# Kernel tuning notes

Measured on AMD Instinct MI355X. Metric: run time of the kernel, lower is better.

## Reference

```python
import jax, jax.numpy as jnp
import numpy as np

B, S, D, H, HID = 4, 1024, 1024, 16, 4096
DK = D // H
EPS = 1e-6


def _ln(x):
    # LayerNorm without affine, eps=1e-6
    mu = jnp.mean(x, axis=-1, keepdims=True)
    var = jnp.var(x, axis=-1, keepdims=True)
    return (x - mu) / jnp.sqrt(var + EPS)


def _lin(x, W, b):
    # torch Linear convention: W is [out, in]
    y = jnp.einsum('...i,oi->...o', x, W)
    return y + b if b is not None else y


def setup_inputs() -> dict:
    key = jax.random.key(0)
    ks = jax.random.split(key, 16)
    sc = lambda fan_in: 1.0 / np.sqrt(fan_in)
    inp = {
        'x': jax.random.normal(ks[0], (B, S, D), jnp.float32),
        'cond': jax.random.normal(ks[1], (B, 1, D), jnp.float32),
        'Wq': jax.random.normal(ks[2], (D, D), jnp.float32) * sc(D),
        'bq': jnp.zeros((D,), jnp.float32),
        'Wk': jax.random.normal(ks[3], (D, D), jnp.float32) * sc(D),
        'bk': jnp.zeros((D,), jnp.float32),
        'Wv': jax.random.normal(ks[4], (D, D), jnp.float32) * sc(D),
        'bv': jnp.zeros((D,), jnp.float32),
        'Wo': jax.random.normal(ks[5], (D, D), jnp.float32) * sc(D),
        'bo': jnp.zeros((D,), jnp.float32),
        'W1': jax.random.normal(ks[6], (HID, D), jnp.float32) * sc(D),
        'b1': jnp.zeros((HID,), jnp.float32),
        'W2': jax.random.normal(ks[7], (D, HID), jnp.float32) * sc(HID),
        'b2': jnp.zeros((D,), jnp.float32),
        'Wada': jax.random.normal(ks[8], (6 * D, D), jnp.float32) * sc(D),
        'bada': jnp.zeros((6 * D,), jnp.float32),
    }
    return inp


def reference(x, cond, Wq, bq, Wk, bk, Wv, bv, Wo, bo, W1, b1, W2, b2, Wada, bada):
    # adaLN modulation: SiLU -> Linear -> chunk 6 along last dim
    mod = _lin(jax.nn.silu(cond), Wada, bada)  # [B,1,6D]
    gama1, beta1, alpha1, gama2, beta2, alpha2 = jnp.split(mod, 6, axis=-1)

    # attention branch
    residual = x
    h = _ln(x) * (1.0 + beta1) + gama1  # modulate(shift=gama1, scale=beta1)
    q = _lin(h, Wq, bq).reshape(B, S, H, DK)
    k = _lin(h, Wk, bk).reshape(B, S, H, DK)
    v = _lin(h, Wv, bv).reshape(B, S, H, DK)
    scores = jnp.einsum('bqhd,bkhd->bhqk', q, k) / jnp.sqrt(jnp.float32(DK))
    probs = jax.nn.softmax(scores, axis=-1)
    attn = jnp.einsum('bhqk,bkhd->bqhd', probs, v).reshape(B, S, D)
    attn = _lin(attn, Wo, bo)
    x = residual + alpha1 * attn

    # MLP branch
    residual = x
    h = _ln(x) * (1.0 + beta2) + gama2
    h = _lin(h, W1, b1)
    h = jax.nn.gelu(h, approximate=False)  # torch nn.GELU default (erf)
    h = _lin(h, W2, b2)
    return residual + alpha2 * h
```

## Files before the change

### kernel.cpp

```cpp
#include <hip/hip_runtime.h>
#include <cstdint>

typedef __bf16 bf16_t;
typedef __bf16 bf16x4 __attribute__((ext_vector_type(4)));
typedef __bf16 bf16x8 __attribute__((ext_vector_type(8)));
typedef float f32x4 __attribute__((ext_vector_type(4)));

#define B_ 4
#define S_ 1024
#define D_ 1024
#define HID_ 4096
#define MEG (1u << 20)

static const size_t OFF_WBF  = 0;
static const size_t OFF_BQKV = 25165824;
static const size_t OFF_MOD  = 25178112;
static const size_t OFF_H    = 25276416;
static const size_t OFF_QKV  = 33665024;
static const size_t OFF_VT   = 58830848;
static const size_t OFF_ATTN = 67219456;
static const size_t OFF_X1   = 75608064;
static const size_t OFF_PART = 92385280;
static const size_t OFF_MLPH = 159494144;

__device__ __forceinline__ void async_copy16(const bf16_t* g, bf16_t* l) {
  __builtin_amdgcn_global_load_lds(
      (__attribute__((address_space(1))) void*)(g),
      (__attribute__((address_space(3))) void*)(l), 16, 0, 0);
}

__global__ __launch_bounds__(256) void convert_pack(
    const float* __restrict__ Wq, const float* __restrict__ Wk,
    const float* __restrict__ Wv, const float* __restrict__ Wo,
    const float* __restrict__ W1, const float* __restrict__ W2,
    const float* __restrict__ bq, const float* __restrict__ bk,
    const float* __restrict__ bv, bf16_t* __restrict__ wbf,
    float* __restrict__ bqkv) {
  const int y = blockIdx.y;
  if (y == 6) {
    int i = blockIdx.x * 256 + threadIdx.x;
    if (i < 3072)
      bqkv[i] = i < 1024 ? bq[i] : (i < 2048 ? bk[i - 1024] : bv[i - 2048]);
    return;
  }
  const float* src; bf16_t* dst; int n;
  switch (y) {
    case 0: src = Wq; dst = wbf;           n = MEG;     break;
    case 1: src = Wk; dst = wbf + MEG;     n = MEG;     break;
    case 2: src = Wv; dst = wbf + 2*MEG;   n = MEG;     break;
    case 3: src = Wo; dst = wbf + 3*MEG;   n = MEG;     break;
    case 4: src = W1; dst = wbf + 4*MEG;   n = 4*MEG;   break;
    default: src = W2; dst = wbf + 8*MEG;  n = 4*MEG;   break;
  }
  int idx = (blockIdx.x * 256 + threadIdx.x) * 4;
  if (idx < n) {
    float4 v = *(const float4*)(src + idx);
    bf16x4 pk;
    pk.x = (__bf16)v.x; pk.y = (__bf16)v.y; pk.z = (__bf16)v.z; pk.w = (__bf16)v.w;
    *(bf16x4*)(dst + idx) = pk;
  }
}

__global__ __launch_bounds__(256) void ada_mod(
    const float* __restrict__ cond, const float* __restrict__ Wada,
    const float* __restrict__ bada, float* __restrict__ mod) {
  const int wave = threadIdx.x >> 6, lane = threadIdx.x & 63;
  const int o = blockIdx.x * 4 + wave;
  const float* wr = Wada + (size_t)o * D_;
  float a0 = 0.f, a1 = 0.f, a2 = 0.f, a3 = 0.f;
#pragma unroll
  for (int l = 0; l < 16; l++) {
    int i = l * 64 + lane;
    float w = wr[i];
    float c0 = cond[i], c1 = cond[1024 + i], c2 = cond[2048 + i], c3 = cond[3072 + i];
    a0 += w * (c0 / (1.0f + __expf(-c0)));
    a1 += w * (c1 / (1.0f + __expf(-c1)));
    a2 += w * (c2 / (1.0f + __expf(-c2)));
    a3 += w * (c3 / (1.0f + __expf(-c3)));
  }
#pragma unroll
  for (int offs = 32; offs; offs >>= 1) {
    a0 += __shfl_xor(a0, offs);
    a1 += __shfl_xor(a1, offs);
    a2 += __shfl_xor(a2, offs);
    a3 += __shfl_xor(a3, offs);
  }
  if (lane == 0) {
    float bb = bada[o];
    mod[o]          = a0 + bb;
    mod[6144 + o]   = a1 + bb;
    mod[12288 + o]  = a2 + bb;
    mod[18432 + o]  = a3 + bb;
  }
}

__global__ __launch_bounds__(256) void ln_modulate(
    const float* __restrict__ X, const float* __restrict__ mod,
    bf16_t* __restrict__ H, int goff) {
  const int row = blockIdx.x;
  const int b = row >> 10;
  const int t = threadIdx.x;
  const float* xr = X + (size_t)row * D_;
  float4 xv = *(const float4*)(xr + t * 4);
  float s = xv.x + xv.y + xv.z + xv.w;
  float q = xv.x*xv.x + xv.y*xv.y + xv.z*xv.z + xv.w*xv.w;
  const int wave = t >> 6, lane = t & 63;
#pragma unroll
  for (int offs = 32; offs; offs >>= 1) {
    s += __shfl_down(s, offs);
    q += __shfl_down(q, offs);
  }
  __shared__ float sb[4][2];
  if (lane == 0) { sb[wave][0] = s; sb[wave][1] = q; }
  __syncthreads();
  float st = sb[0][0] + sb[1][0] + sb[2][0] + sb[3][0];
  float qt = sb[0][1] + sb[1][1] + sb[2][1] + sb[3][1];
  float mu = st * (1.0f / D_);
  float var = qt * (1.0f / D_) - mu * mu;
  float rstd = rsqrtf(var + 1e-6f);
  const float* mb = mod + (size_t)b * 6144 + goff;
  const int c = t * 4;
  float4 gm = *(const float4*)(mb + c);
  float4 bt = *(const float4*)(mb + 1024 + c);
  bf16x4 pk;
  pk.x = (__bf16)((xv.x - mu) * rstd * (1.0f + bt.x) + gm.x);
  pk.y = (__bf16)((xv.y - mu) * rstd * (1.0f + bt.y) + gm.y);
  pk.z = (__bf16)((xv.z - mu) * rstd * (1.0f + bt.z) + gm.z);
  pk.w = (__bf16)((xv.w - mu) * rstd * (1.0f + bt.w) + gm.w);
  *(bf16x4*)(H + (size_t)row * D_ + c) = pk;
}

__global__ __launch_bounds__(256) void transpose_v(
    const bf16_t* __restrict__ qkv, bf16_t* __restrict__ vT) {
  __shared__ bf16_t tile[64][65];
  const int bh = blockIdx.y;
  const int b = bh >> 4, hh = bh & 15;
  const int s0 = blockIdx.x * 64;
  const int t = threadIdx.x;
  const int tx = t & 63, ty = t >> 6;
  const bf16_t* src = qkv + (size_t)b * S_ * 3072 + 2048 + hh * 64;
  for (int r = ty; r < 64; r += 4)
    tile[r][tx] = src[(size_t)(s0 + r) * 3072 + tx];
  __syncthreads();
  bf16_t* dst = vT + (size_t)bh * 64 * 1024;
  for (int r = ty; r < 64; r += 4)
    dst[(size_t)r * 1024 + s0 + tx] = tile[tx][r];
}

__global__ __launch_bounds__(256) void flash_attn(
    const bf16_t* __restrict__ qkv, const bf16_t* __restrict__ vT,
    bf16_t* __restrict__ attn) {
  __shared__ __align__(16) bf16_t Qs[64 * 64];
  __shared__ __align__(16) bf16_t Ks[128 * 64];
  __shared__ __align__(16) bf16_t Vs[64 * 128];
  __shared__ __align__(16) bf16_t Ps[4 * 16 * 136];

  const int t = threadIdx.x;
  const int wave = t >> 6, lane = t & 63;
  const int lm = lane & 15, quad = lane >> 4;
  const int bh = blockIdx.y;
  const int b = bh >> 4, hh = bh & 15;
  const int s0 = blockIdx.x * 64;

  const bf16_t* qbase = qkv + (size_t)b * S_ * 3072 + hh * 64;
  const bf16_t* kbase = qbase + 1024;
  const bf16_t* vbase = vT + (size_t)bh * (64 * 1024);

#pragma unroll
  for (int j = 0; j < 2; j++) {
    int slot = j * 256 + t;
    int row = slot >> 3;
    int cg = (slot & 7) ^ (row & 7);
    async_copy16(qbase + (size_t)(s0 + row) * 3072 + cg * 8, &Qs[slot * 8]);
  }

  f32x4 accO[4] = {};
  float mrow[4], lrow[4];
#pragma unroll
  for (int r = 0; r < 4; r++) { mrow[r] = -1e30f; lrow[r] = 0.f; }

  bf16_t* Pw = &Ps[wave * 16 * 136];

  for (int k0 = 0; k0 < S_; k0 += 128) {
    __syncthreads();
#pragma unroll
    for (int j = 0; j < 4; j++) {
      int slot = j * 256 + t;
      int row = slot >> 3;
      int cg = (slot & 7) ^ (row & 7);
      async_copy16(kbase + (size_t)(k0 + row) * 3072 + cg * 8, &Ks[slot * 8]);
    }
#pragma unroll
    for (int j = 0; j < 4; j++) {
      int slot = j * 256 + t;
      int row = slot >> 4;
      int cp = slot & 15;
      int cg = (cp & 8) | ((cp & 7) ^ (row & 7));
      async_copy16(vbase + (size_t)row * 1024 + k0 + cg * 8, &Vs[slot * 8]);
    }
    __syncthreads();

    f32x4 accS[8] = {};
#pragma unroll
    for (int ks = 0; ks < 2; ks++) {
      int rq = wave * 16 + lm;
      int cq = (ks * 4 + quad) ^ (rq & 7);
      bf16x8 aq = *(const bf16x8*)&Qs[rq * 64 + cq * 8];
#pragma unroll
      for (int ni = 0; ni < 8; ni++) {
        int rk = ni * 16 + lm;
        int ck = (ks * 4 + quad) ^ (rk & 7);
        bf16x8 bk8 = *(const bf16x8*)&Ks[rk * 64 + ck * 8];
        accS[ni] = __builtin_amdgcn_mfma_f32_16x16x32_bf16(aq, bk8, accS[ni], 0, 0, 0);
      }
    }

    float alpha[4];
#pragma unroll
    for (int r = 0; r < 4; r++) {
      float mx = accS[0][r];
#pragma unroll
      for (int ni = 1; ni < 8; ni++) mx = fmaxf(mx, accS[ni][r]);
      mx = fmaxf(mx, __shfl_xor(mx, 1));
      mx = fmaxf(mx, __shfl_xor(mx, 2));
      mx = fmaxf(mx, __shfl_xor(mx, 4));
      mx = fmaxf(mx, __shfl_xor(mx, 8));
      mx *= 0.125f;
      float mnew = fmaxf(mrow[r], mx);
      alpha[r] = __expf(mrow[r] - mnew);
      mrow[r] = mnew;
      float sum = 0.f;
#pragma unroll
      for (int ni = 0; ni < 8; ni++) {
        float p = __expf(accS[ni][r] * 0.125f - mnew);
        accS[ni][r] = p;
        sum += p;
      }
      sum += __shfl_xor(sum, 1);
      sum += __shfl_xor(sum, 2);
      sum += __shfl_xor(sum, 4);
      sum += __shfl_xor(sum, 8);
      lrow[r] = lrow[r] * alpha[r] + sum;
    }
#pragma unroll
    for (int di = 0; di < 4; di++)
#pragma unroll
      for (int r = 0; r < 4; r++) accO[di][r] *= alpha[r];

#pragma unroll
    for (int ni = 0; ni < 8; ni++)
#pragma unroll
      for (int r = 0; r < 4; r++)
        Pw[(quad * 4 + r) * 136 + ni * 16 + lm] = (__bf16)accS[ni][r];

#pragma unroll
    for (int ks2 = 0; ks2 < 4; ks2++) {
      bf16x8 ap = *(const bf16x8*)&Pw[lm * 136 + ks2 * 32 + quad * 8];
#pragma unroll
      for (int di = 0; di < 4; di++) {
        int rv = di * 16 + lm;
        int g = ks2 * 4 + quad;
        int cp = (g & 8) | ((g & 7) ^ (rv & 7));
        bf16x8 bv = *(const bf16x8*)&Vs[rv * 128 + cp * 8];
        accO[di] = __builtin_amdgcn_mfma_f32_16x16x32_bf16(ap, bv, accO[di], 0, 0, 0);
      }
    }
  }

#pragma unroll
  for (int r = 0; r < 4; r++) {
    float inv = 1.0f / lrow[r];
    int row = quad * 4 + r;
#pragma unroll
    for (int di = 0; di < 4; di++) {
      int col = di * 16 + lm;
      int cph = (col >> 3) ^ (row & 7);
      Pw[row * 64 + cph * 8 + (col & 7)] = (__bf16)(accO[di][r] * inv);
    }
  }
  bf16_t* abase = attn + (size_t)b * S_ * 1024 +
                  (size_t)(s0 + wave * 16) * 1024 + hh * 64;
#pragma unroll
  for (int it = 0; it < 2; it++) {
    int slot = it * 64 + lane;
    int row = slot >> 3;
    int cg = slot & 7;
    int cph = cg ^ (row & 7);
    bf16x8 val = *(const bf16x8*)&Pw[row * 64 + cph * 8];
    *(bf16x8*)(abase + (size_t)row * 1024 + cg * 8) = val;
  }
}

template <int EPI>
__global__ __launch_bounds__(256) void gemm_bt(
    const bf16_t* __restrict__ A, int lda, long long sAz,
    const bf16_t* __restrict__ B, int ldb, long long sBz,
    void* __restrict__ Cv, int ldc, long long sCz,
    int M, int N, int K,
    const float* __restrict__ bias,
    float scale) {
  __shared__ __align__(16) bf16_t As[2][128 * 32];
  __shared__ __align__(16) bf16_t Bs[2][128 * 32];

  const int z = blockIdx.z;
  A += (size_t)z * sAz;
  B += (size_t)z * sBz;

  {
    int d = blockIdx.x + gridDim.x * blockIdx.y;
    int xcd = d & 7, sId = d >> 3;
    int qq = sId & 31, panel = sId >> 5;
    const int bx = panel * 8 + (qq >> 2);
    const int by = xcd * 4 + (qq & 3);
    const int t = threadIdx.x;
    const int wave = t >> 6;
    const int lane = t & 63;
    const int lm = lane & 15;
    const int quad = lane >> 4;
    const int wr = wave >> 1;
    const int wc = wave & 1;

    const int m0 = by * 128;
    const int n0 = bx * 128;

    f32x4 acc[4][4] = {};

    const int srow = t >> 2;
    const int gch = (t & 3) ^ ((srow >> 1) & 3);
    const int lds_off = t * 8;
    const bf16_t* Ap0 = A + (size_t)(m0 + srow) * lda + gch * 8;
    const bf16_t* Ap1 = A + (size_t)(m0 + 64 + srow) * lda + gch * 8;
    const bf16_t* Bp0 = B + (size_t)(n0 + srow) * ldb + gch * 8;
    const bf16_t* Bp1 = B + (size_t)(n0 + 64 + srow) * ldb + gch * 8;

    const int sOff = (quad ^ ((lm >> 1) & 3)) * 8;

    const int niter = K >> 5;
    async_copy16(Ap0, &As[0][lds_off]);
    async_copy16(Ap1, &As[0][2048 + lds_off]);
    async_copy16(Bp0, &Bs[0][lds_off]);
    async_copy16(Bp1, &Bs[0][2048 + lds_off]);

    for (int it = 0; it < niter; ++it) {
      asm volatile("s_waitcnt vmcnt(0)\n\ts_barrier" ::: "memory");
      if (it + 1 < niter) {
        const int ko = (it + 1) << 5;
        const int nb = (it + 1) & 1;
        async_copy16(Ap0 + ko, &As[nb][lds_off]);
        async_copy16(Ap1 + ko, &As[nb][2048 + lds_off]);
        async_copy16(Bp0 + ko, &Bs[nb][lds_off]);
        async_copy16(Bp1 + ko, &Bs[nb][2048 + lds_off]);
      }
      const int cb = it & 1;
      bf16x8 af[4], bfr[4];
#pragma unroll
      for (int i = 0; i < 4; i++) {
        af[i] = *(const bf16x8*)&As[cb][(wr * 64 + i * 16 + lm) * 32 + sOff];
        bfr[i] = *(const bf16x8*)&Bs[cb][(wc * 64 + i * 16 + lm) * 32 + sOff];
      }
#pragma unroll
      for (int mi = 0; mi < 4; mi++)
#pragma unroll
        for (int ni = 0; ni < 4; ni++)
          acc[mi][ni] = __builtin_amdgcn_mfma_f32_16x16x32_bf16(
              af[mi], bfr[ni], acc[mi][ni], 0, 0, 0);
    }

    const size_t cz = (size_t)z * sCz;
#pragma unroll
    for (int mi = 0; mi < 4; mi++) {
#pragma unroll
      for (int ni = 0; ni < 4; ni++) {
#pragma unroll
        for (int r = 0; r < 4; r++) {
          int row = m0 + wr * 64 + mi * 16 + quad * 4 + r;
          int col = n0 + wc * 64 + ni * 16 + lm;
          float v = acc[mi][ni][r];
          size_t idx = cz + (size_t)row * ldc + col;
          if (EPI == 1) {
            ((float*)Cv)[idx] = v * scale;
          } else if (EPI == 0) {
            if (bias) v += bias[col];
            ((bf16_t*)Cv)[idx] = (__bf16)v;
          } else if (EPI == 3) {
            v += bias[col];
            float u = 1.5957691216f * (v + 0.044715f * v * v * v);
            float g = v / (1.0f + __expf(-u));
            ((bf16_t*)Cv)[idx] = (__bf16)g;
          }
        }
      }
    }
  }
}

__global__ __launch_bounds__(256) void reduce_ln(
    const float* __restrict__ part, const float* __restrict__ x,
    const float* __restrict__ bo, const float* __restrict__ mod,
    float* __restrict__ x1, bf16_t* __restrict__ h) {
  const int row = blockIdx.x;
  const int b = row >> 10;
  const int t = threadIdx.x;
  const int c = t * 4;
  const size_t idx = (size_t)row * 1024 + c;
  float4 p0 = *(const float4*)(part + idx);
  float4 p1 = *(const float4*)(part + 4194304 + idx);
  float4 bb = *(const float4*)(bo + c);
  float4 al = *(const float4*)(mod + (size_t)b * 6144 + 2048 + c);
  float4 xs = *(const float4*)(x + idx);
  float4 xv;
  xv.x = xs.x + al.x * (p0.x + p1.x + bb.x);
  xv.y = xs.y + al.y * (p0.y + p1.y + bb.y);
  xv.z = xs.z + al.z * (p0.z + p1.z + bb.z);
  xv.w = xs.w + al.w * (p0.w + p1.w + bb.w);
  *(float4*)(x1 + idx) = xv;

  float s = xv.x + xv.y + xv.z + xv.w;
  float q = xv.x*xv.x + xv.y*xv.y + xv.z*xv.z + xv.w*xv.w;
  const int wave = t >> 6, lane = t & 63;
#pragma unroll
  for (int offs = 32; offs; offs >>= 1) {
    s += __shfl_down(s, offs);
    q += __shfl_down(q, offs);
  }
  __shared__ float sb[4][2];
  if (lane == 0) { sb[wave][0] = s; sb[wave][1] = q; }
  __syncthreads();
  float st = sb[0][0] + sb[1][0] + sb[2][0] + sb[3][0];
  float qt = sb[0][1] + sb[1][1] + sb[2][1] + sb[3][1];
  float mu = st * (1.0f / D_);
  float var = qt * (1.0f / D_) - mu * mu;
  float rstd = rsqrtf(var + 1e-6f);
  const float* mb = mod + (size_t)b * 6144 + 3072;
  float4 gm = *(const float4*)(mb + c);
  float4 bt = *(const float4*)(mb + 1024 + c);
  bf16x4 pk;
  pk.x = (__bf16)((xv.x - mu) * rstd * (1.0f + bt.x) + gm.x);
  pk.y = (__bf16)((xv.y - mu) * rstd * (1.0f + bt.y) + gm.y);
  pk.z = (__bf16)((xv.z - mu) * rstd * (1.0f + bt.z) + gm.z);
  pk.w = (__bf16)((xv.w - mu) * rstd * (1.0f + bt.w) + gm.w);
  *(bf16x4*)(h + idx) = pk;
}

__global__ __launch_bounds__(256) void reduce_w2(
    const float* __restrict__ part, const float* __restrict__ x1,
    const float* __restrict__ b2, const float* __restrict__ mod,
    float* __restrict__ out) {
  const int idx = (blockIdx.x * 256 + threadIdx.x) * 4;
  const int col = idx & 1023;
  const int row = idx >> 10;
  const int b = row >> 10;
  float4 s0 = *(const float4*)(part + idx);
  float4 s1 = *(const float4*)(part + 4194304 + idx);
  float4 bb = *(const float4*)(b2 + col);
  float4 al = *(const float4*)(mod + (size_t)b * 6144 + 5120 + col);
  float4 rs = *(const float4*)(x1 + idx);
  float4 o;
  o.x = rs.x + al.x * (s0.x + s1.x + bb.x);
  o.y = rs.y + al.y * (s0.y + s1.y + bb.y);
  o.z = rs.z + al.z * (s0.z + s1.z + bb.z);
  o.w = rs.w + al.w * (s0.w + s1.w + bb.w);
  *(float4*)(out + idx) = o;
}

extern "C" void kernel_launch(void* const* d_in, const int* in_sizes, int n_in,
                              void* d_out, int out_size, void* d_ws, size_t ws_size,
                              hipStream_t stream) {
  (void)in_sizes; (void)n_in; (void)out_size; (void)ws_size;
  const float* x    = (const float*)d_in[0];
  const float* cond = (const float*)d_in[1];
  const float* Wq   = (const float*)d_in[2];
  const float* bq   = (const float*)d_in[3];
  const float* Wk   = (const float*)d_in[4];
  const float* bk   = (const float*)d_in[5];
  const float* Wv   = (const float*)d_in[6];
  const float* bv   = (const float*)d_in[7];
  const float* Wo   = (const float*)d_in[8];
  const float* bo   = (const float*)d_in[9];
  const float* W1   = (const float*)d_in[10];
  const float* b1   = (const float*)d_in[11];
  const float* W2   = (const float*)d_in[12];
  const float* b2   = (const float*)d_in[13];
  const float* Wada = (const float*)d_in[14];
  const float* bada = (const float*)d_in[15];

  uint8_t* ws = (uint8_t*)d_ws;
  bf16_t* wbf   = (bf16_t*)(ws + OFF_WBF);
  float*  bqkv  = (float*)(ws + OFF_BQKV);
  float*  mod   = (float*)(ws + OFF_MOD);
  bf16_t* h     = (bf16_t*)(ws + OFF_H);
  bf16_t* qkv   = (bf16_t*)(ws + OFF_QKV);
  bf16_t* vT    = (bf16_t*)(ws + OFF_VT);
  bf16_t* attn  = (bf16_t*)(ws + OFF_ATTN);
  float*  x1    = (float*)(ws + OFF_X1);
  float*  part  = (float*)(ws + OFF_PART);
  bf16_t* mlph  = (bf16_t*)(ws + OFF_MLPH);
  float* out = (float*)d_out;

  convert_pack<<<dim3(4096, 7, 1), 256, 0, stream>>>(Wq, Wk, Wv, Wo, W1, W2,
                                                     bq, bk, bv, wbf, bqkv);
  ada_mod<<<1536, 256, 0, stream>>>(cond, Wada, bada, mod);
  ln_modulate<<<4096, 256, 0, stream>>>(x, mod, h, 0);
  gemm_bt<0><<<dim3(24, 32, 1), 256, 0, stream>>>(
      h, 1024, 0, wbf, 1024, 0, qkv, 3072, 0, 4096, 3072, 1024,
      bqkv, 1.f);
  transpose_v<<<dim3(16, 64, 1), 256, 0, stream>>>(qkv, vT);
  flash_attn<<<dim3(16, 64, 1), 256, 0, stream>>>(qkv, vT, attn);

  gemm_bt<1><<<dim3(8, 32, 2), 256, 0, stream>>>(
      attn, 1024, 512, wbf + (size_t)3 * MEG, 1024, 512, part, 1024, 4194304,
      4096, 1024, 512, nullptr, 1.f);
  reduce_ln<<<4096, 256, 0, stream>>>(part, x, bo, mod, x1, h);

  gemm_bt<3><<<dim3(32, 32, 1), 256, 0, stream>>>(
      h, 1024, 0, wbf + (size_t)4 * MEG, 1024, 0, mlph, 4096, 0,
      4096, 4096, 1024, b1, 1.f);
  gemm_bt<1><<<dim3(8, 32, 2), 256, 0, stream>>>(
      mlph, 4096, 2048, wbf + (size_t)8 * MEG, 4096, 2048, part, 1024, 4194304,
      4096, 1024, 2048, nullptr, 1.f);
  reduce_w2<<<4096, 256, 0, stream>>>(part, x1, b2, mod, out);
}
```

Measured before the change: 408.8 us.

## Double-buffer K/V tiles in flash attention with register-resident Q and exp2 softmax

Restructures the flash attention kernel to use 64-key tiles with double-buffered K and V shared memory, prefetching the next tile while computing the current one, with one barrier per iteration. Q is loaded once into registers, reusing the shared buffer. The softmax now uses exp2 with a folded log2(e)/sqrt(dk) scale, and s_setprio is raised around the MFMA blocks. Shared memory per block shrinks and launch bounds request 4 blocks per CU, aiming at higher occupancy and better load/compute overlap, at the cost of more loop iterations and synchronisations.

```diff
diff --git a/kernel.cpp b/kernel.cpp
--- a/kernel.cpp
+++ b/kernel.cpp
@@ -147,13 +147,12 @@
     dst[(size_t)r * 1024 + s0 + tx] = tile[tx][r];
 }
 
-__global__ __launch_bounds__(256) void flash_attn(
+__global__ __launch_bounds__(256, 4) void flash_attn(
     const bf16_t* __restrict__ qkv, const bf16_t* __restrict__ vT,
     bf16_t* __restrict__ attn) {
-  __shared__ __align__(16) bf16_t Qs[64 * 64];
-  __shared__ __align__(16) bf16_t Ks[128 * 64];
-  __shared__ __align__(16) bf16_t Vs[64 * 128];
-  __shared__ __align__(16) bf16_t Ps[4 * 16 * 136];
+  __shared__ __align__(16) bf16_t Ks[2][64 * 64];
+  __shared__ __align__(16) bf16_t Vs[2][64 * 64];
+  __shared__ __align__(16) bf16_t Ps[4][16 * 64];
 
   const int t = threadIdx.x;
   const int wave = t >> 6, lane = t & 63;
@@ -166,73 +165,75 @@
   const bf16_t* kbase = qbase + 1024;
   const bf16_t* vbase = vT + (size_t)bh * (64 * 1024);
 
-#pragma unroll
-  for (int j = 0; j < 2; j++) {
-    int slot = j * 256 + t;
-    int row = slot >> 3;
-    int cg = (slot & 7) ^ (row & 7);
-    async_copy16(qbase + (size_t)(s0 + row) * 3072 + cg * 8, &Qs[slot * 8]);
-  }
+  const int row0 = t >> 3;
+  const int cg = (t & 7) ^ (row0 & 7);
+  const int o0 = t * 8, o1 = 2048 + t * 8;
+
+  async_copy16(qbase + (size_t)(s0 + row0) * 3072 + cg * 8, &Ks[1][o0]);
+  async_copy16(qbase + (size_t)(s0 + 32 + row0) * 3072 + cg * 8, &Ks[1][o1]);
+  async_copy16(kbase + (size_t)row0 * 3072 + cg * 8, &Ks[0][o0]);
+  async_copy16(kbase + (size_t)(32 + row0) * 3072 + cg * 8, &Ks[0][o1]);
+  async_copy16(vbase + (size_t)row0 * 1024 + cg * 8, &Vs[0][o0]);
+  async_copy16(vbase + (size_t)(32 + row0) * 1024 + cg * 8, &Vs[0][o1]);
+  __syncthreads();
+
+  bf16x8 aq0, aq1;
+  {
+    const int rq = wave * 16 + lm;
+    const int rb = lm & 7;
+    aq0 = *(const bf16x8*)&Ks[1][rq * 64 + (quad ^ rb) * 8];
+    aq1 = *(const bf16x8*)&Ks[1][rq * 64 + ((4 + quad) ^ rb) * 8];
+  }
+  __syncthreads();
 
   f32x4 accO[4] = {};
   float mrow[4], lrow[4];
 #pragma unroll
   for (int r = 0; r < 4; r++) { mrow[r] = -1e30f; lrow[r] = 0.f; }
 
-  bf16_t* Pw = &Ps[wave * 16 * 136];
-
-  for (int k0 = 0; k0 < S_; k0 += 128) {
-    __syncthreads();
-#pragma unroll
-    for (int j = 0; j < 4; j++) {
-      int slot = j * 256 + t;
-      int row = slot >> 3;
-      int cg = (slot & 7) ^ (row & 7);
-      async_copy16(kbase + (size_t)(k0 + row) * 3072 + cg * 8, &Ks[slot * 8]);
-    }
-#pragma unroll
-    for (int j = 0; j < 4; j++) {
-      int slot = j * 256 + t;
-      int row = slot >> 4;
-      int cp = slot & 15;
-      int cg = (cp & 8) | ((cp & 7) ^ (row & 7));
-      async_copy16(vbase + (size_t)row * 1024 + k0 + cg * 8, &Vs[slot * 8]);
-    }
-    __syncthreads();
-
-    f32x4 accS[8] = {};
-#pragma unroll
-    for (int ks = 0; ks < 2; ks++) {
-      int rq = wave * 16 + lm;
-      int cq = (ks * 4 + quad) ^ (rq & 7);
-      bf16x8 aq = *(const bf16x8*)&Qs[rq * 64 + cq * 8];
-#pragma unroll
-      for (int ni = 0; ni < 8; ni++) {
-        int rk = ni * 16 + lm;
-        int ck = (ks * 4 + quad) ^ (rk & 7);
-        bf16x8 bk8 = *(const bf16x8*)&Ks[rk * 64 + ck * 8];
-        accS[ni] = __builtin_amdgcn_mfma_f32_16x16x32_bf16(aq, bk8, accS[ni], 0, 0, 0);
-      }
-    }
+  const float SC = 0.18033688f;
+  bf16_t* Pw = Ps[wave];
+  const int rb = lm & 7;
+
+  for (int tt = 0; tt < 16; ++tt) {
+    const int cur = tt & 1;
+    if (tt < 15) {
+      const int nb = cur ^ 1;
+      const int k0n = (tt + 1) << 6;
+      async_copy16(kbase + (size_t)(k0n + row0) * 3072 + cg * 8, &Ks[nb][o0]);
+      async_copy16(kbase + (size_t)(k0n + 32 + row0) * 3072 + cg * 8, &Ks[nb][o1]);
+      async_copy16(vbase + (size_t)row0 * 1024 + k0n + cg * 8, &Vs[nb][o0]);
+      async_copy16(vbase + (size_t)(32 + row0) * 1024 + k0n + cg * 8, &Vs[nb][o1]);
+    }
+
+    f32x4 accS[4] = {};
+    __builtin_amdgcn_s_setprio(1);
+#pragma unroll
+    for (int ni = 0; ni < 4; ni++) {
+      const int rk = ni * 16 + lm;
+      bf16x8 b0 = *(const bf16x8*)&Ks[cur][rk * 64 + ((quad ^ rb)) * 8];
+      bf16x8 b1 = *(const bf16x8*)&Ks[cur][rk * 64 + (((4 + quad) ^ rb)) * 8];
+      accS[ni] = __builtin_amdgcn_mfma_f32_16x16x32_bf16(aq0, b0, accS[ni], 0, 0, 0);
+      accS[ni] = __builtin_amdgcn_mfma_f32_16x16x32_bf16(aq1, b1, accS[ni], 0, 0, 0);
+    }
+    __builtin_amdgcn_s_setprio(0);
 
     float alpha[4];
 #pragma unroll
     for (int r = 0; r < 4; r++) {
-      float mx = accS[0][r];
-#pragma unroll
-      for (int ni = 1; ni < 8; ni++) mx = fmaxf(mx, accS[ni][r]);
+      float mx = fmaxf(fmaxf(accS[0][r], accS[1][r]),
+                       fmaxf(accS[2][r], accS[3][r])) * SC;
       mx = fmaxf(mx, __shfl_xor(mx, 1));
       mx = fmaxf(mx, __shfl_xor(mx, 2));
       mx = fmaxf(mx, __shfl_xor(mx, 4));
       mx = fmaxf(mx, __shfl_xor(mx, 8));
-      mx *= 0.125f;
       float mnew = fmaxf(mrow[r], mx);
-      alpha[r] = __expf(mrow[r] - mnew);
+      alpha[r] = exp2f(mrow[r] - mnew);
       mrow[r] = mnew;
       float sum = 0.f;
 #pragma unroll
-      for (int ni = 0; ni < 8; ni++) {
-        float p = __expf(accS[ni][r] * 0.125f - mnew);
+      for (int ni = 0; ni < 4; ni++) {
+        float p = exp2f(accS[ni][r] * SC - mnew);
         accS[ni][r] = p;
         sum += p;
       }
@@ -248,34 +249,41 @@
       for (int r = 0; r < 4; r++) accO[di][r] *= alpha[r];
 
 #pragma unroll
-    for (int ni = 0; ni < 8; ni++)
-#pragma unroll
-      for (int r = 0; r < 4; r++)
-        Pw[(quad * 4 + r) * 136 + ni * 16 + lm] = (__bf16)accS[ni][r];
-
-#pragma unroll
-    for (int ks2 = 0; ks2 < 4; ks2++) {
-      bf16x8 ap = *(const bf16x8*)&Pw[lm * 136 + ks2 * 32 + quad * 8];
+    for (int ni = 0; ni < 4; ni++)
+#pragma unroll
+      for (int r = 0; r < 4; r++) {
+        int prow = quad * 4 + r;
+        int col = ni * 16 + lm;
+        Pw[prow * 64 + (((col >> 3) ^ (prow & 7)) << 3) + (col & 7)] =
+            (__bf16)accS[ni][r];
+      }
+
+    {
+      bf16x8 ap0 = *(const bf16x8*)&Pw[lm * 64 + ((quad ^ rb)) * 8];
+      bf16x8 ap1 = *(const bf16x8*)&Pw[lm * 64 + (((4 + quad) ^ rb)) * 8];
+      __builtin_amdgcn_s_setprio(1);
 #pragma unroll
       for (int di = 0; di < 4; di++) {
-        int rv = di * 16 + lm;
-        int g = ks2 * 4 + quad;
-        int cp = (g & 8) | ((g & 7) ^ (rv & 7));
-        bf16x8 bv = *(const bf16x8*)&Vs[rv * 128 + cp * 8];
-        accO[di] = __builtin_amdgcn_mfma_f32_16x16x32_bf16(ap, bv, accO[di], 0, 0, 0);
+        const int rv = di * 16 + lm;
+        bf16x8 v0 = *(const bf16x8*)&Vs[cur][rv * 64 + ((quad ^ rb)) * 8];
+        bf16x8 v1 = *(const bf16x8*)&Vs[cur][rv * 64 + (((4 + quad) ^ rb)) * 8];
+        accO[di] = __builtin_amdgcn_mfma_f32_16x16x32_bf16(ap0, v0, accO[di], 0, 0, 0);
+        accO[di] = __builtin_amdgcn_mfma_f32_16x16x32_bf16(ap1, v1, accO[di], 0, 0, 0);
       }
-    }
+      __builtin_amdgcn_s_setprio(0);
+    }
+    __syncthreads();
   }
 
 #pragma unroll
   for (int r = 0; r < 4; r++) {
     float inv = 1.0f / lrow[r];
-    int row = quad * 4 + r;
+    int prow = quad * 4 + r;
 #pragma unroll
     for (int di = 0; di < 4; di++) {
       int col = di * 16 + lm;
-      int cph = (col >> 3) ^ (row & 7);
-      Pw[row * 64 + cph * 8 + (col & 7)] = (__bf16)(accO[di][r] * inv);
+      int cph = (col >> 3) ^ (prow & 7);
+      Pw[prow * 64 + cph * 8 + (col & 7)] = (__bf16)(accO[di][r] * inv);
     }
   }
   bf16_t* abase = attn + (size_t)b * S_ * 1024 +
@@ -283,11 +291,11 @@
 #pragma unroll
   for (int it = 0; it < 2; it++) {
     int slot = it * 64 + lane;
-    int row = slot >> 3;
-    int cg = slot & 7;
-    int cph = cg ^ (row & 7);
-    bf16x8 val = *(const bf16x8*)&Pw[row * 64 + cph * 8];
-    *(bf16x8*)(abase + (size_t)row * 1024 + cg * 8) = val;
+    int orow = slot >> 3;
+    int gc = slot & 7;
+    int cph = gc ^ (orow & 7);
+    bf16x8 val = *(const bf16x8*)&Pw[orow * 64 + cph * 8];
+    *(bf16x8*)(abase + (size_t)orow * 1024 + gc * 8) = val;
   }
 }
 
```

Measured after the change: 406.2 us. Within noise of the previous version (-0.6%).
